# Kernel tuning notes

Hardware: AMD Instinct MI355X
Metric: run time of the kernel (lower is better)

The kernel has to match this reference:

```python
import jax, jax.numpy as jnp
import numpy as np

K = 16          # neighbors per query (args.k)
EPS_NORM = 1e-5  # LayerNorm / BatchNorm eps (torch default)


def _knn_edges(xyz, B, n):
    # batch-aware kNN: equal-sized batches, edges never cross batch boundary
    x = xyz.reshape(B, n, 3)
    d2 = jnp.sum((x[:, :, None, :] - x[:, None, :, :]) ** 2, -1)   # [B,n,n]
    _, idx = jax.lax.top_k(-d2, K)                                 # [B,n,K] local neighbor ids
    col = (idx + (jnp.arange(B) * n)[:, None, None]).reshape(-1)   # source (neighbor) [E]
    row = jnp.repeat(jnp.arange(B * n), K)                         # target (query)    [E]
    return row, col


def _forward(support_xyz, batch_index, features, lang_features, mask_flattened,
             W1, b1, ln_g, ln_b, W2, b2,
             Wl1, bl1, bn_g, bn_b, Wl2, bl2,
             Wr1, br1, Wr2, br2, row, col):
    N = support_xyz.shape[0]
    B, L, Fl = lang_features.shape
    # feat_encoder: Linear -> LayerNorm -> ReLU -> Linear
    h = features @ W1 + b1
    mu = h.mean(-1, keepdims=True)
    var = ((h - mu) ** 2).mean(-1, keepdims=True)
    h = (h - mu) / jnp.sqrt(var + EPS_NORM) * ln_g + ln_b
    feats = jax.nn.relu(h) @ W2 + b2                               # [N,F]
    # lang_encoder: Linear -> BatchNorm1d (batch statistics) -> ReLU -> Linear
    hl = lang_features.reshape(B * L, Fl) @ Wl1 + bl1
    mul = hl.mean(0)
    varl = ((hl - mul) ** 2).mean(0)
    hl = (hl - mul) / jnp.sqrt(varl + EPS_NORM) * bn_g + bn_b
    lang = (jax.nn.relu(hl) @ Wl2 + bl2).reshape(B, L, -1)         # [B,L,F]
    lang_flat = lang[batch_index]                                  # [N,L,F]
    # per-point / per-token attention logits
    atten = jnp.einsum('nf,nlf->nl', feats, lang_flat)             # [N,L]
    # segment softmax over incoming kNN edges (CenterOp max / add)
    attenmax = jax.ops.segment_max(atten[col], row, num_segments=N, indices_are_sorted=True)
    a = jnp.exp(atten[col] - attenmax[row])                        # [E,L]
    attensum = jax.ops.segment_sum(a, row, num_segments=N, indices_are_sorted=True)
    # CenterConv message
    att = a / attensum[row] * mask_flattened[row]                  # [E,L]
    att = att / (att.sum(-1, keepdims=True) + 1e-7)
    ctx = jnp.einsum('el,elf->ef', att, lang_flat[col])            # [E,F] attended lang feat
    xi, xj = support_xyz[row], support_xyz[col]
    d = xi - xj
    nrm = jnp.sqrt(jnp.sum(d * d, -1, keepdims=True) + 1e-12)
    ew = jnp.concatenate([xi, xj, d, nrm], -1)                     # [E,10]
    ew = jax.nn.relu(ew @ Wr1 + br1) @ Wr2 + br2                   # [E,F] rel_encoder
    msg = feats[col] * ctx * ew                                    # [E,F]
    rel = jax.ops.segment_sum(msg, row, num_segments=N, indices_are_sorted=True)
    return feats + rel


def setup_inputs() -> dict:
    key = jax.random.key(0)
    ks = jax.random.split(key, 12)
    B, n, L = 4, 1024, 16
    N = B * n
    Fv, Fl, F = 256, 768, 128
    def w(k, shp, fan):
        return jax.random.normal(k, shp, jnp.float32) / np.sqrt(fan).astype(np.float32)
    mask = (jax.random.uniform(ks[3], (N, L)) < 0.8).astype(jnp.float32).at[:, 0].set(1.0)
    return {
        'support_xyz': jax.random.normal(ks[0], (N, 3), jnp.float32),
        'batch_index': jnp.repeat(jnp.arange(B), n),
        'features': jax.random.normal(ks[1], (N, Fv), jnp.float32),
        'lang_features': jax.random.normal(ks[2], (B, L, Fl), jnp.float32),
        'mask_flattened': mask,
        'W1': w(ks[4], (Fv, F), Fv), 'b1': jnp.zeros(F, jnp.float32),
        'ln_g': jnp.ones(F, jnp.float32), 'ln_b': jnp.zeros(F, jnp.float32),
        'W2': w(ks[5], (F, F), F), 'b2': jnp.zeros(F, jnp.float32),
        'Wl1': w(ks[6], (Fl, F), Fl), 'bl1': jnp.zeros(F, jnp.float32),
        'bn_g': jnp.ones(F, jnp.float32), 'bn_b': jnp.zeros(F, jnp.float32),
        'Wl2': w(ks[7], (F, F), F), 'bl2': jnp.zeros(F, jnp.float32),
        'Wr1': w(ks[8], (10, 64), 10), 'br1': jnp.zeros(64, jnp.float32),
        'Wr2': w(ks[9], (64, F), 64), 'br2': jnp.zeros(F, jnp.float32),
    }


def reference(support_xyz, batch_index, features, lang_features, mask_flattened,
              W1, b1, ln_g, ln_b, W2, b2,
              Wl1, bl1, bn_g, bn_b, Wl2, bl2,
              Wr1, br1, Wr2, br2):
    B = lang_features.shape[0]
    n = support_xyz.shape[0] // B
    row, col = _knn_edges(support_xyz, B, n)
    return _forward(support_xyz, batch_index, features, lang_features, mask_flattened,
                    W1, b1, ln_g, ln_b, W2, b2,
                    Wl1, bl1, bn_g, bn_b, Wl2, bl2,
                    Wr1, br1, Wr2, br2, row, col)
```

## Files before the change

### kernel.cpp

```cpp
#include <hip/hip_runtime.h>

typedef unsigned long long u64;
typedef unsigned int u32;
typedef short short8 __attribute__((ext_vector_type(8)));
typedef float f32x4 __attribute__((ext_vector_type(4)));
typedef u32 u32x4v __attribute__((ext_vector_type(4)));

#define N_PTS   4096
#define B_SZ    4
#define N_PER_B 1024
#define L_TOK   16
#define FV      256
#define FL      768
#define FDIM    128
#define KNN     16
#define RH      64

#define MFMA_BF16(a, b, c) __builtin_amdgcn_mfma_f32_16x16x32_bf16((a), (b), (c), 0, 0, 0)

__device__ __forceinline__ short f2bf(float f) {
    unsigned int x = __float_as_uint(f);
    unsigned int r = (x + 0x7fffu + ((x >> 16) & 1u)) >> 16;
    return (short)r;
}

__global__ __launch_bounds__(256) void k1_kernel(const float* __restrict__ xyz,
                                                 const float* __restrict__ features,
                                                 const float* __restrict__ lf,
                                                 const float* __restrict__ Wl1,
                                                 const float* __restrict__ bl1,
                                                 const float* __restrict__ W1,
                                                 const float* __restrict__ W2,
                                                 int* __restrict__ knn,
                                                 float* __restrict__ hl,
                                                 short* __restrict__ fp_hi,
                                                 short* __restrict__ fp_lo,
                                                 short* __restrict__ w1p_hi,
                                                 short* __restrict__ w1p_lo,
                                                 short* __restrict__ w2p_hi,
                                                 short* __restrict__ w2p_lo) {
    __shared__ float smem[1024];
    int b = blockIdx.x, t = threadIdx.x;

    if (b < 1024) {
        int lane = t & 63;
        int q = b * 4 + (t >> 6);
        int base = (q >> 10) << 10;
        float qx = xyz[q * 3 + 0];
        float qy = xyz[q * 3 + 1];
        float qz = xyz[q * 3 + 2];
        u64 keys[16];
#pragma unroll
        for (int m = 0; m < 16; m++) {
            int j = base + lane + (m << 6);
            float dx = qx - xyz[j * 3 + 0];
            float dy = qy - xyz[j * 3 + 1];
            float dz = qz - xyz[j * 3 + 2];
            float d2 = __fadd_rn(__fadd_rn(__fmul_rn(dx, dx), __fmul_rn(dy, dy)),
                                 __fmul_rn(dz, dz));
            keys[m] = (((u64)__float_as_uint(d2)) << 32) | (unsigned int)j;
        }
        for (int r = 0; r < KNN; r++) {
            u64 lmin = keys[0];
#pragma unroll
            for (int m = 1; m < 16; m++) lmin = (keys[m] < lmin) ? keys[m] : lmin;
            u64 g = lmin;
#pragma unroll
            for (int off = 32; off > 0; off >>= 1) {
                u64 o = __shfl_xor(g, off, 64);
                g = (o < g) ? o : g;
            }
#pragma unroll
            for (int m = 0; m < 16; m++)
                if (keys[m] == g) keys[m] = ~0ULL;
            if (lane == 0) knn[q * KNN + r] = (int)(g & 0xffffffffu);
        }
    } else if (b < 1088) {
        int r = b - 1024;
        float* lrow = smem;
        float* part = smem + 768;
        for (int k = t; k < FL; k += 256) lrow[k] = lf[r * FL + k];
        __syncthreads();
        int c = t & 127, kh = t >> 7;
        float acc = (kh == 0) ? bl1[c] : 0.f;
        int k0 = kh * 384;
        for (int k = k0; k < k0 + 384; k++) acc += lrow[k] * Wl1[k * FDIM + c];
        part[kh * FDIM + c] = acc;
        __syncthreads();
        if (kh == 0) hl[r * FDIM + c] = part[c] + part[FDIM + c];
    } else if (b < 1344) {
        int rt = b - 1088;
        int lane = t & 63, kh = t >> 6;
        int e = lane & 15, q = lane >> 4;
#pragma unroll
        for (int pp = 0; pp < 2; pp++) {
            int ks = kh * 2 + pp;
            const float* src = features + (rt * 16 + e) * FV + ks * 32 + q * 8;
            float4 f0 = *(const float4*)src;
            float4 f1 = *(const float4*)(src + 4);
            float f[8] = {f0.x, f0.y, f0.z, f0.w, f1.x, f1.y, f1.z, f1.w};
            short8 hi, lo;
#pragma unroll
            for (int j = 0; j < 8; j++) {
                u32 bits = __float_as_uint(f[j]);
                hi[j] = (short)(bits >> 16);
                float lof = f[j] - __uint_as_float(bits & 0xffff0000u);
                lo[j] = (short)(__float_as_uint(lof) >> 16);
            }
            int o = ((rt * 8 + ks) * 64 + lane) * 8;
            *(short8*)(fp_hi + o) = hi;
            *(short8*)(fp_lo + o) = lo;
        }
    } else {
        int isW2 = (b >= 1352);
        int ks = isW2 ? (b - 1352) : (b - 1344);
        const float* W = isW2 ? W2 : W1;
        short* ph = isW2 ? w2p_hi : w1p_hi;
        short* pl = isW2 ? w2p_lo : w1p_lo;
        int lane = t & 63, cth = t >> 6;
        int e = lane & 15, q = lane >> 4;
#pragma unroll
        for (int p = 0; p < 2; p++) {
            int ct = cth * 2 + p;
            short8 hi, lo;
#pragma unroll
            for (int j = 0; j < 8; j++) {
                float w = W[(ks * 32 + q * 8 + j) * FDIM + ct * 16 + e];
                u32 bits = __float_as_uint(w);
                hi[j] = (short)(bits >> 16);
                float lof = w - __uint_as_float(bits & 0xffff0000u);
                lo[j] = (short)(__float_as_uint(lof) >> 16);
            }
            int o = ((ks * 8 + ct) * 64 + lane) * 8;
            *(short8*)(ph + o) = hi;
            *(short8*)(pl + o) = lo;
        }
    }
}

__global__ __launch_bounds__(256) void k2_kernel(const short* __restrict__ fp_hi,
                                                 const short* __restrict__ fp_lo,
                                                 const short* __restrict__ w1p_hi,
                                                 const short* __restrict__ w1p_lo,
                                                 const short* __restrict__ w2p_hi,
                                                 const short* __restrict__ w2p_lo,
                                                 const float* __restrict__ b1,
                                                 const float* __restrict__ ln_g,
                                                 const float* __restrict__ ln_b,
                                                 const float* __restrict__ b2,
                                                 const float* __restrict__ hl,
                                                 const float* __restrict__ bn_g,
                                                 const float* __restrict__ bn_b,
                                                 const float* __restrict__ Wl2,
                                                 const float* __restrict__ bl2,
                                                 float* __restrict__ feats,
                                                 float* __restrict__ lang) {
    int b = blockIdx.x, t = threadIdx.x;
    if (b < 64) {
        __shared__ u32 hbuf[4][16 * 132];
        int wid = t >> 6, lane = t & 63;
        int e = lane & 15, q = lane >> 4;
        int rt = b * 4 + wid;

        f32x4 acc[8];
#pragma unroll
        for (int ct = 0; ct < 8; ct++) {
            float v = b1[ct * 16 + e];
            acc[ct] = (f32x4){v, v, v, v};
        }
        for (int ks = 0; ks < 8; ks++) {
            int ao = ((rt * 8 + ks) * 64 + lane) * 8;
            short8 ah = *(const short8*)(fp_hi + ao);
            short8 al = *(const short8*)(fp_lo + ao);
#pragma unroll
            for (int ct = 0; ct < 8; ct++) {
                int bo = ((ks * 8 + ct) * 64 + lane) * 8;
                short8 bh = *(const short8*)(w1p_hi + bo);
                short8 bl = *(const short8*)(w1p_lo + bo);
                acc[ct] = MFMA_BF16(ah, bh, acc[ct]);
                acc[ct] = MFMA_BF16(al, bh, acc[ct]);
                acc[ct] = MFMA_BF16(ah, bl, acc[ct]);
            }
        }
        float s[4], sq[4];
#pragma unroll
        for (int r = 0; r < 4; r++) { s[r] = 0.f; sq[r] = 0.f; }
#pragma unroll
        for (int ct = 0; ct < 8; ct++)
#pragma unroll
            for (int r = 0; r < 4; r++) {
                float v = acc[ct][r];
                s[r] += v; sq[r] += v * v;
            }
#pragma unroll
        for (int off = 1; off < 16; off <<= 1)
#pragma unroll
            for (int r = 0; r < 4; r++) {
                s[r] += __shfl_xor(s[r], off, 16);
                sq[r] += __shfl_xor(sq[r], off, 16);
            }
        float mu[4], rs[4];
#pragma unroll
        for (int r = 0; r < 4; r++) {
            mu[r] = s[r] * (1.f / 128.f);
            float var = sq[r] * (1.f / 128.f) - mu[r] * mu[r];
            rs[r] = rsqrtf(var + 1e-5f);
        }
        u32* hrow = &hbuf[wid][0];
#pragma unroll
        for (int ct = 0; ct < 8; ct++) {
            float g = ln_g[ct * 16 + e], bb = ln_b[ct * 16 + e];
#pragma unroll
            for (int r = 0; r < 4; r++) {
                float n = fmaxf((acc[ct][r] - mu[r]) * rs[r] * g + bb, 0.f);
                u32 nb = __float_as_uint(n);
                u32 hh = nb & 0xffff0000u;
                float lof = n - __uint_as_float(hh);
                hrow[(q * 4 + r) * 132 + ct * 16 + e] = hh | (__float_as_uint(lof) >> 16);
            }
        }
        f32x4 acc2[8];
#pragma unroll
        for (int ct = 0; ct < 8; ct++) {
            float v = b2[ct * 16 + e];
            acc2[ct] = (f32x4){v, v, v, v};
        }
#pragma unroll
        for (int ks = 0; ks < 4; ks++) {
            u32 hv[8];
            *(u32x4v*)&hv[0] = *(const u32x4v*)&hrow[e * 132 + ks * 32 + q * 8];
            *(u32x4v*)&hv[4] = *(const u32x4v*)&hrow[e * 132 + ks * 32 + q * 8 + 4];
            short8 ah, al;
#pragma unroll
            for (int j = 0; j < 8; j++) {
                ah[j] = (short)(hv[j] >> 16);
                al[j] = (short)(hv[j] & 0xffffu);
            }
#pragma unroll
            for (int ct = 0; ct < 8; ct++) {
                int bo = ((ks * 8 + ct) * 64 + lane) * 8;
                short8 bh = *(const short8*)(w2p_hi + bo);
                short8 bl = *(const short8*)(w2p_lo + bo);
                acc2[ct] = MFMA_BF16(ah, bh, acc2[ct]);
                acc2[ct] = MFMA_BF16(al, bh, acc2[ct]);
                acc2[ct] = MFMA_BF16(ah, bl, acc2[ct]);
            }
        }
#pragma unroll
        for (int ct = 0; ct < 8; ct++)
#pragma unroll
            for (int r = 0; r < 4; r++)
                feats[(rt * 16 + q * 4 + r) * FDIM + ct * 16 + e] = acc2[ct][r];
    } else {
        __shared__ float rl4[4][FDIM];
        int tt = t & 127;
        int act = (t < 128);
        int r0 = (b - 64) * 4;
        if (act) {
            float s = 0.f, s2 = 0.f;
            for (int r = 0; r < 64; r++) {
                float v = hl[r * FDIM + tt];
                s += v; s2 += v * v;
            }
            float mu = s * (1.f / 64.f);
            float var = s2 * (1.f / 64.f) - mu * mu;
            float rs = rsqrtf(var + 1e-5f);
            float g = bn_g[tt], bb = bn_b[tt];
#pragma unroll
            for (int p = 0; p < 4; p++)
                rl4[p][tt] = fmaxf((hl[(r0 + p) * FDIM + tt] - mu) * rs * g + bb, 0.f);
        }
        __syncthreads();
        if (act) {
            float bv = bl2[tt];
            float a0 = bv, a1 = bv, a2 = bv, a3 = bv;
            for (int k = 0; k < FDIM; k++) {
                float w = Wl2[k * FDIM + tt];
                a0 += rl4[0][k] * w;
                a1 += rl4[1][k] * w;
                a2 += rl4[2][k] * w;
                a3 += rl4[3][k] * w;
            }
            lang[(r0 + 0) * FDIM + tt] = a0;
            lang[(r0 + 1) * FDIM + tt] = a1;
            lang[(r0 + 2) * FDIM + tt] = a2;
            lang[(r0 + 3) * FDIM + tt] = a3;
        }
    }
}

__global__ __launch_bounds__(256) void atten_kernel(const float* __restrict__ feats,
                                                    const float* __restrict__ lang,
                                                    float* __restrict__ atten) {
    __shared__ float fb[2][FDIM];
    __shared__ float pb[256];
    int t = threadIdx.x;
    int half = t >> 7, tt = t & 127;
    int i = blockIdx.x * 2 + half;
    fb[half][tt] = feats[i * FDIM + tt];
    __syncthreads();
    int l = tt >> 3, sj = tt & 7;
    int bi = i >> 10;
    const float* lrow = lang + (bi * L_TOK + l) * FDIM;
    float p = 0.f;
#pragma unroll
    for (int m = 0; m < 16; m++) {
        int k = sj + (m << 3);
        p += fb[half][k] * lrow[k];
    }
    pb[t] = p;
    __syncthreads();
    if (tt < L_TOK) {
        float a = 0.f;
#pragma unroll
        for (int u = 0; u < 8; u++) a += pb[half * 128 + tt * 8 + u];
        atten[i * L_TOK + tt] = a;
    }
}

__global__ __launch_bounds__(256) void edge_kernel(const float* __restrict__ xyz,
                                                   const float* __restrict__ mask,
                                                   const float* __restrict__ Wr1,
                                                   const float* __restrict__ br1,
                                                   const float* __restrict__ Wr2,
                                                   const float* __restrict__ br2,
                                                   const int* __restrict__ knn,
                                                   const float* __restrict__ lang,
                                                   const float* __restrict__ feats,
                                                   const float* __restrict__ atten,
                                                   float* __restrict__ out) {
    int lane = threadIdx.x & 63;
    int wid  = threadIdx.x >> 6;
    int i    = blockIdx.x * 4 + wid;
    int bi   = i >> 10;
    int quad = lane >> 4;
    int e16  = lane & 15;

    int idxe = knn[i * KNN + e16];

    float sat[8];
    if (quad < 2) {
        const float4* ap = (const float4*)(atten + idxe * L_TOK + quad * 8);
        float4 a0 = ap[0], a1 = ap[1];
        sat[0] = a0.x; sat[1] = a0.y; sat[2] = a0.z; sat[3] = a0.w;
        sat[4] = a1.x; sat[5] = a1.y; sat[6] = a1.z; sat[7] = a1.w;
    } else {
#pragma unroll
        for (int j = 0; j < 8; j++) sat[j] = 0.f;
    }

    float mx[8];
#pragma unroll
    for (int j = 0; j < 8; j++) mx[j] = sat[j];
#pragma unroll
    for (int off = 1; off < 16; off <<= 1) {
#pragma unroll
        for (int j = 0; j < 8; j++) mx[j] = fmaxf(mx[j], __shfl_xor(mx[j], off, 16));
    }
    float ex[8], sm[8];
#pragma unroll
    for (int j = 0; j < 8; j++) { ex[j] = __expf(sat[j] - mx[j]); sm[j] = ex[j]; }
#pragma unroll
    for (int off = 1; off < 16; off <<= 1) {
#pragma unroll
        for (int j = 0; j < 8; j++) sm[j] += __shfl_xor(sm[j], off, 16);
    }
    float st[8];
    if (quad < 2) {
        const float4* mp = (const float4*)(mask + i * L_TOK + quad * 8);
        float4 m0 = mp[0], m1 = mp[1];
        float mv[8] = {m0.x, m0.y, m0.z, m0.w, m1.x, m1.y, m1.z, m1.w};
#pragma unroll
        for (int j = 0; j < 8; j++) st[j] = ex[j] * (mv[j] / sm[j]);
    } else {
#pragma unroll
        for (int j = 0; j < 8; j++) st[j] = 0.f;
    }
    float s = st[0] + st[1] + st[2] + st[3] + st[4] + st[5] + st[6] + st[7];
    s += __shfl_xor(s, 16, 64);
    s += __shfl_xor(s, 32, 64);
    float inv2 = 1.f / (s + 1e-7f);
    short8 sattA;
#pragma unroll
    for (int j = 0; j < 8; j++) sattA[j] = f2bf(st[j] * inv2);

    float xi0 = xyz[i * 3 + 0], xi1 = xyz[i * 3 + 1], xi2 = xyz[i * 3 + 2];
    float xj0 = xyz[idxe * 3 + 0], xj1 = xyz[idxe * 3 + 1], xj2 = xyz[idxe * 3 + 2];
    float d0 = xi0 - xj0, d1 = xi1 - xj1, d2v = xi2 - xj2;
    float nr = sqrtf(d0 * d0 + d1 * d1 + d2v * d2v + 1e-12f);
    float ein[10] = {xi0, xi1, xi2, xj0, xj1, xj2, d0, d1, d2v, nr};
    short8 hidA[2];
#pragma unroll
    for (int sstep = 0; sstep < 2; sstep++) {
        int k0 = sstep * 32 + quad * 8;
        float h[8];
        const float4* bp = (const float4*)(br1 + k0);
        float4 b0 = bp[0], b1v = bp[1];
        h[0] = b0.x; h[1] = b0.y; h[2] = b0.z; h[3] = b0.w;
        h[4] = b1v.x; h[5] = b1v.y; h[6] = b1v.z; h[7] = b1v.w;
#pragma unroll
        for (int m = 0; m < 10; m++) {
            const float4* wp = (const float4*)(Wr1 + m * RH + k0);
            float4 w0 = wp[0], w1 = wp[1];
            float em = ein[m];
            h[0] += em * w0.x; h[1] += em * w0.y; h[2] += em * w0.z; h[3] += em * w0.w;
            h[4] += em * w1.x; h[5] += em * w1.y; h[6] += em * w1.z; h[7] += em * w1.w;
        }
#pragma unroll
        for (int j = 0; j < 8; j++) hidA[sstep][j] = f2bf(fmaxf(h[j], 0.f));
    }

    int idxr[4];
#pragma unroll
    for (int r = 0; r < 4; r++) idxr[r] = knn[i * KNN + quad * 4 + r];

#pragma unroll 2
    for (int tile = 0; tile < 8; tile++) {
        int cc = tile * 16 + e16;
        f32x4 accew = {0.f, 0.f, 0.f, 0.f};
#pragma unroll
        for (int sstep = 0; sstep < 2; sstep++) {
            short8 w2B;
#pragma unroll
            for (int j = 0; j < 8; j++)
                w2B[j] = f2bf(Wr2[(sstep * 32 + quad * 8 + j) * FDIM + cc]);
            accew = __builtin_amdgcn_mfma_f32_16x16x32_bf16(hidA[sstep], w2B, accew, 0, 0, 0);
        }
        short8 lsB;
        if (quad < 2) {
#pragma unroll
            for (int j = 0; j < 8; j++)
                lsB[j] = f2bf(lang[bi * L_TOK * FDIM + (quad * 8 + j) * FDIM + cc]);
        } else {
#pragma unroll
            for (int j = 0; j < 8; j++) lsB[j] = 0;
        }
        f32x4 accctx = {0.f, 0.f, 0.f, 0.f};
        accctx = __builtin_amdgcn_mfma_f32_16x16x32_bf16(sattA, lsB, accctx, 0, 0, 0);

        float br2c = br2[cc];
        float msum = 0.f;
#pragma unroll
        for (int r = 0; r < 4; r++) {
            float fj = feats[idxr[r] * FDIM + cc];
            msum += fj * accctx[r] * (accew[r] + br2c);
        }
        msum += __shfl_xor(msum, 16, 64);
        msum += __shfl_xor(msum, 32, 64);
        if (lane < 16)
            out[i * FDIM + cc] = feats[i * FDIM + cc] + msum;
    }
}

extern "C" void kernel_launch(void* const* d_in, const int* in_sizes, int n_in,
                              void* d_out, int out_size, void* d_ws, size_t ws_size,
                              hipStream_t stream) {
    const float* xyz   = (const float*)d_in[0];
    const float* features = (const float*)d_in[2];
    const float* lang_f   = (const float*)d_in[3];
    const float* mask     = (const float*)d_in[4];
    const float* W1   = (const float*)d_in[5];
    const float* b1   = (const float*)d_in[6];
    const float* ln_g = (const float*)d_in[7];
    const float* ln_b = (const float*)d_in[8];
    const float* W2   = (const float*)d_in[9];
    const float* b2   = (const float*)d_in[10];
    const float* Wl1  = (const float*)d_in[11];
    const float* bl1  = (const float*)d_in[12];
    const float* bn_g = (const float*)d_in[13];
    const float* bn_b = (const float*)d_in[14];
    const float* Wl2  = (const float*)d_in[15];
    const float* bl2  = (const float*)d_in[16];
    const float* Wr1  = (const float*)d_in[17];
    const float* br1  = (const float*)d_in[18];
    const float* Wr2  = (const float*)d_in[19];
    const float* br2  = (const float*)d_in[20];

    float* ws_feats = (float*)d_ws;
    float* ws_atten = ws_feats + N_PTS * FDIM;
    float* ws_lang  = ws_atten + N_PTS * L_TOK;
    float* ws_hl    = ws_lang + B_SZ * L_TOK * FDIM;
    int*   ws_knn   = (int*)(ws_hl + 64 * FDIM);
    short* fp_hi    = (short*)(ws_knn + N_PTS * KNN);
    short* fp_lo    = fp_hi + N_PTS * FV;
    short* w1p_hi   = fp_lo + N_PTS * FV;
    short* w1p_lo   = w1p_hi + FV * FDIM;
    short* w2p_hi   = w1p_lo + FV * FDIM;
    short* w2p_lo   = w2p_hi + FDIM * FDIM;

    k1_kernel<<<1356, 256, 0, stream>>>(xyz, features, lang_f, Wl1, bl1, W1, W2,
                                        ws_knn, ws_hl,
                                        fp_hi, fp_lo, w1p_hi, w1p_lo, w2p_hi, w2p_lo);
    k2_kernel<<<80, 256, 0, stream>>>(fp_hi, fp_lo, w1p_hi, w1p_lo, w2p_hi, w2p_lo,
                                      b1, ln_g, ln_b, b2,
                                      ws_hl, bn_g, bn_b, Wl2, bl2,
                                      ws_feats, ws_lang);
    atten_kernel<<<N_PTS / 2, 256, 0, stream>>>(ws_feats, ws_lang, ws_atten);
    edge_kernel<<<N_PTS / 4, 256, 0, stream>>>(xyz, mask, Wr1, br1, Wr2, br2,
                                               ws_knn, ws_lang, ws_feats, ws_atten,
                                               (float*)d_out);
}
```

Before: 164.1 us.

## Replace iterative kNN argmin with bitonic sort-merge and prepack edge MFMA operands

```diff
diff --git a/kernel.cpp b/kernel.cpp
--- a/kernel.cpp
+++ b/kernel.cpp
@@ -31,6 +31,7 @@
                                                  const float* __restrict__ bl1,
                                                  const float* __restrict__ W1,
                                                  const float* __restrict__ W2,
+                                                 const float* __restrict__ Wr2,
                                                  int* __restrict__ knn,
                                                  float* __restrict__ hl,
                                                  short* __restrict__ fp_hi,
@@ -38,7 +39,8 @@
                                                  short* __restrict__ w1p_hi,
                                                  short* __restrict__ w1p_lo,
                                                  short* __restrict__ w2p_hi,
-                                                 short* __restrict__ w2p_lo) {
+                                                 short* __restrict__ w2p_lo,
+                                                 short* __restrict__ w2pe) {
     __shared__ float smem[1024];
     int b = blockIdx.x, t = threadIdx.x;
 
@@ -49,31 +51,66 @@
         float qx = xyz[q * 3 + 0];
         float qy = xyz[q * 3 + 1];
         float qz = xyz[q * 3 + 2];
-        u64 keys[16];
+        double key[16];
 #pragma unroll
         for (int m = 0; m < 16; m++) {
-            int j = base + lane + (m << 6);
+            int jl = lane + (m << 6);
+            int j = base + jl;
             float dx = qx - xyz[j * 3 + 0];
             float dy = qy - xyz[j * 3 + 1];
             float dz = qz - xyz[j * 3 + 2];
             float d2 = __fadd_rn(__fadd_rn(__fmul_rn(dx, dx), __fmul_rn(dy, dy)),
                                  __fmul_rn(dz, dz));
-            keys[m] = (((u64)__float_as_uint(d2)) << 32) | (unsigned int)j;
-        }
-        for (int r = 0; r < KNN; r++) {
-            u64 lmin = keys[0];
-#pragma unroll
-            for (int m = 1; m < 16; m++) lmin = (keys[m] < lmin) ? keys[m] : lmin;
-            u64 g = lmin;
-#pragma unroll
-            for (int off = 32; off > 0; off >>= 1) {
-                u64 o = __shfl_xor(g, off, 64);
-                g = (o < g) ? o : g;
-            }
-#pragma unroll
-            for (int m = 0; m < 16; m++)
-                if (keys[m] == g) keys[m] = ~0ULL;
-            if (lane == 0) knn[q * KNN + r] = (int)(g & 0xffffffffu);
+            key[m] = (double)__float_as_uint(d2) * 1024.0 + (double)jl;
+        }
+#pragma unroll
+        for (int k = 2; k <= 16; k <<= 1) {
+#pragma unroll
+            for (int jj = k >> 1; jj > 0; jj >>= 1) {
+#pragma unroll
+                for (int i = 0; i < 16; i++) {
+                    int l = i ^ jj;
+                    if (l > i) {
+                        double lo = fmin(key[i], key[l]);
+                        double hi = fmax(key[i], key[l]);
+                        bool asc = ((i & k) == 0);
+                        key[i] = asc ? lo : hi;
+                        key[l] = asc ? hi : lo;
+                    }
+                }
+            }
+        }
+#pragma unroll
+        for (int lvl = 1; lvl <= 32; lvl <<= 1) {
+            double pk[16];
+#pragma unroll
+            for (int i = 0; i < 16; i++) pk[i] = __shfl_xor(key[15 - i], lvl, 64);
+#pragma unroll
+            for (int i = 0; i < 16; i++) key[i] = fmin(key[i], pk[i]);
+#pragma unroll
+            for (int jj = 8; jj > 0; jj >>= 1) {
+#pragma unroll
+                for (int i = 0; i < 16; i++) {
+                    int l = i ^ jj;
+                    if (l > i) {
+                        double lo = fmin(key[i], key[l]);
+                        double hi = fmax(key[i], key[l]);
+                        key[i] = lo;
+                        key[l] = hi;
+                    }
+                }
+            }
+        }
+        if (lane == 0) {
+            int idx[16];
+#pragma unroll
+            for (int i = 0; i < 16; i++)
+                idx[i] = base + (int)(((u64)key[i]) & 1023u);
+#pragma unroll
+            for (int w = 0; w < 4; w++) {
+                int4 v = {idx[4 * w], idx[4 * w + 1], idx[4 * w + 2], idx[4 * w + 3]};
+                *(int4*)&knn[q * KNN + 4 * w] = v;
+            }
         }
     } else if (b < 1088) {
         int r = b - 1024;
@@ -111,7 +148,7 @@
             *(short8*)(fp_hi + o) = hi;
             *(short8*)(fp_lo + o) = lo;
         }
-    } else {
+    } else if (b < 1356) {
         int isW2 = (b >= 1352);
         int ks = isW2 ? (b - 1352) : (b - 1344);
         const float* W = isW2 ? W2 : W1;
@@ -134,6 +171,19 @@
             int o = ((ks * 8 + ct) * 64 + lane) * 8;
             *(short8*)(ph + o) = hi;
             *(short8*)(pl + o) = lo;
+        }
+    } else {
+        int ks = b - 1356;
+        int lane = t & 63, cth = t >> 6;
+        int e = lane & 15, q = lane >> 4;
+#pragma unroll
+        for (int p = 0; p < 2; p++) {
+            int ct = cth * 2 + p;
+            short8 v;
+#pragma unroll
+            for (int j = 0; j < 8; j++)
+                v[j] = f2bf(Wr2[(ks * 32 + q * 8 + j) * FDIM + ct * 16 + e]);
+            *(short8*)(w2pe + ((ks * 8 + ct) * 64 + lane) * 8) = v;
         }
     }
 }
@@ -291,30 +341,52 @@
 
 __global__ __launch_bounds__(256) void atten_kernel(const float* __restrict__ feats,
                                                     const float* __restrict__ lang,
-                                                    float* __restrict__ atten) {
-    __shared__ float fb[2][FDIM];
-    __shared__ float pb[256];
+                                                    float* __restrict__ atten,
+                                                    short* __restrict__ langp) {
     int t = threadIdx.x;
-    int half = t >> 7, tt = t & 127;
-    int i = blockIdx.x * 2 + half;
-    fb[half][tt] = feats[i * FDIM + tt];
-    __syncthreads();
-    int l = tt >> 3, sj = tt & 7;
-    int bi = i >> 10;
-    const float* lrow = lang + (bi * L_TOK + l) * FDIM;
-    float p = 0.f;
-#pragma unroll
-    for (int m = 0; m < 16; m++) {
-        int k = sj + (m << 3);
-        p += fb[half][k] * lrow[k];
-    }
-    pb[t] = p;
-    __syncthreads();
-    if (tt < L_TOK) {
-        float a = 0.f;
-#pragma unroll
-        for (int u = 0; u < 8; u++) a += pb[half * 128 + tt * 8 + u];
-        atten[i * L_TOK + tt] = a;
+    int b = blockIdx.x;
+    if (b < 2048) {
+        __shared__ float fb[2][FDIM];
+        __shared__ float pb[256];
+        int half = t >> 7, tt = t & 127;
+        int i = b * 2 + half;
+        fb[half][tt] = feats[i * FDIM + tt];
+        __syncthreads();
+        int l = tt >> 3, sj = tt & 7;
+        int bi = i >> 10;
+        const float* lrow = lang + (bi * L_TOK + l) * FDIM;
+        float p = 0.f;
+#pragma unroll
+        for (int m = 0; m < 16; m++) {
+            int k = sj + (m << 3);
+            p += fb[half][k] * lrow[k];
+        }
+        pb[t] = p;
+        __syncthreads();
+        if (tt < L_TOK) {
+            float a = 0.f;
+#pragma unroll
+            for (int u = 0; u < 8; u++) a += pb[half * 128 + tt * 8 + u];
+            atten[i * L_TOK + tt] = a;
+        }
+    } else {
+        int bi = b - 2048;
+        int lane = t & 63, w = t >> 6;
+        int e = lane & 15, qd = lane >> 4;
+#pragma unroll
+        for (int p = 0; p < 2; p++) {
+            int tile = w * 2 + p;
+            short8 v;
+            if (qd < 2) {
+#pragma unroll
+                for (int j = 0; j < 8; j++)
+                    v[j] = f2bf(lang[bi * L_TOK * FDIM + (qd * 8 + j) * FDIM + tile * 16 + e]);
+            } else {
+#pragma unroll
+                for (int j = 0; j < 8; j++) v[j] = 0;
+            }
+            *(short8*)(langp + ((bi * 8 + tile) * 64 + lane) * 8) = v;
+        }
     }
 }
 
@@ -322,10 +394,10 @@
                                                    const float* __restrict__ mask,
                                                    const float* __restrict__ Wr1,
                                                    const float* __restrict__ br1,
-                                                   const float* __restrict__ Wr2,
                                                    const float* __restrict__ br2,
                                                    const int* __restrict__ knn,
-                                                   const float* __restrict__ lang,
+                                                   const short* __restrict__ w2pe,
+                                                   const short* __restrict__ langp,
                                                    const float* __restrict__ feats,
                                                    const float* __restrict__ atten,
                                                    float* __restrict__ out) {
@@ -420,21 +492,10 @@
         f32x4 accew = {0.f, 0.f, 0.f, 0.f};
 #pragma unroll
         for (int sstep = 0; sstep < 2; sstep++) {
-            short8 w2B;
-#pragma unroll
-            for (int j = 0; j < 8; j++)
-                w2B[j] = f2bf(Wr2[(sstep * 32 + quad * 8 + j) * FDIM + cc]);
+            short8 w2B = *(const short8*)(w2pe + ((sstep * 8 + tile) * 64 + lane) * 8);
             accew = __builtin_amdgcn_mfma_f32_16x16x32_bf16(hidA[sstep], w2B, accew, 0, 0, 0);
         }
-        short8 lsB;
-        if (quad < 2) {
-#pragma unroll
-            for (int j = 0; j < 8; j++)
-                lsB[j] = f2bf(lang[bi * L_TOK * FDIM + (quad * 8 + j) * FDIM + cc]);
-        } else {
-#pragma unroll
-            for (int j = 0; j < 8; j++) lsB[j] = 0;
-        }
+        short8 lsB = *(const short8*)(langp + ((bi * 8 + tile) * 64 + lane) * 8);
         f32x4 accctx = {0.f, 0.f, 0.f, 0.f};
         accctx = __builtin_amdgcn_mfma_f32_16x16x32_bf16(sattA, lsB, accctx, 0, 0, 0);
 
@@ -487,16 +548,19 @@
     short* w1p_lo   = w1p_hi + FV * FDIM;
     short* w2p_hi   = w1p_lo + FV * FDIM;
     short* w2p_lo   = w2p_hi + FDIM * FDIM;
-
-    k1_kernel<<<1356, 256, 0, stream>>>(xyz, features, lang_f, Wl1, bl1, W1, W2,
+    short* w2pe     = w2p_lo + FDIM * FDIM;
+    short* langp    = w2pe + RH * FDIM;
+
+    k1_kernel<<<1358, 256, 0, stream>>>(xyz, features, lang_f, Wl1, bl1, W1, W2, Wr2,
                                         ws_knn, ws_hl,
-                                        fp_hi, fp_lo, w1p_hi, w1p_lo, w2p_hi, w2p_lo);
+                                        fp_hi, fp_lo, w1p_hi, w1p_lo, w2p_hi, w2p_lo,
+                                        w2pe);
     k2_kernel<<<80, 256, 0, stream>>>(fp_hi, fp_lo, w1p_hi, w1p_lo, w2p_hi, w2p_lo,
                                       b1, ln_g, ln_b, b2,
                                       ws_hl, bn_g, bn_b, Wl2, bl2,
                                       ws_feats, ws_lang);
-    atten_kernel<<<N_PTS / 2, 256, 0, stream>>>(ws_feats, ws_lang, ws_atten);
-    edge_kernel<<<N_PTS / 4, 256, 0, stream>>>(xyz, mask, Wr1, br1, Wr2, br2,
-                                               ws_knn, ws_lang, ws_feats, ws_atten,
+    atten_kernel<<<2052, 256, 0, stream>>>(ws_feats, ws_lang, ws_atten, langp);
+    edge_kernel<<<N_PTS / 4, 256, 0, stream>>>(xyz, mask, Wr1, br1, br2,
+                                               ws_knn, w2pe, langp, ws_feats, ws_atten,
                                                (float*)d_out);
 }
```

New measurement: 156.1 us. 1.05x faster.
